# Kernel tuning notes

Hardware: AMD Instinct MI355X
Metric: run time of the kernel (lower is better)

## Reference

```python
import jax, jax.numpy as jnp
import numpy as np

N, B, T = 2048, 16, 256

def setup_inputs() -> dict:
    key = jax.random.key(0)
    k1, k2, k3, k4 = jax.random.split(key, 4)
    x = jax.random.normal(k1, (B, T, N), dtype=jnp.float32)
    weight = jax.random.normal(k2, (T, T), dtype=jnp.float32) * (1.0 / np.sqrt(T))
    bias = jax.random.normal(k3, (T,), dtype=jnp.float32) * 0.01
    # Gumbel(0,1) noise, matching torch.nn.functional.gumbel_softmax internals
    u = jax.random.uniform(k4, (N * N, 2), dtype=jnp.float32, minval=1e-6, maxval=1.0 - 1e-6)
    gumbel = -jnp.log(-jnp.log(u))
    return {"x": x, "weight": weight, "bias": bias, "gumbel": gumbel}

def reference(x, weight, bias, gumbel):
    # x: [B, T, N] -> node-major [N, B, T]
    xp = jnp.transpose(x, (2, 0, 1))
    n = xp.shape[0]
    # --- similarity-based logits (torch writes via .data -> no grad path) ---
    xs = jax.lax.stop_gradient(xp)
    x_avg = xs.mean(axis=1)                                          # [N, T]
    x_norm = x_avg / jnp.maximum(jnp.linalg.norm(x_avg, axis=-1, keepdims=True), 1e-12)
    sim = (x_norm @ x_norm.T + 1.0) * 0.5                            # [N, N] in [0,1]
    sim_flat = sim.reshape(-1)
    # gumbel_softmax(hard=True) forward: adjacency = argmax over (logits + g)
    score0 = sim_flat + gumbel[:, 0]
    score1 = (1.0 - sim_flat) + gumbel[:, 1]
    adj = (score0 > score1).astype(xp.dtype).reshape(n, n)           # directed adjacency
    # --- structural coefficient (dense, faithful to compute_structural_coeff) ---
    adj_sym = jnp.clip(adj + adj.T, 0.0, 1.0)
    nmask = jnp.clip(adj_sym + jnp.eye(n, dtype=xp.dtype), 0.0, 1.0)
    common = nmask @ nmask.T                                         # common-neighbor counts
    max_common = common.max()                                        # >= 1 (diagonal)
    valid = (adj_sym * (common > 1.0).astype(xp.dtype)) > 0
    struct = jnp.where(valid, (common / max_common) * common, 0.0)   # lambda_val = 1.0
    # edge weights only at directed-edge positions
    W = adj * struct                                                 # [src, dst]
    # --- gcn_norm (no self loops, improved=False): deg over dst, D^-1/2 W D^-1/2 ---
    deg = W.sum(axis=0)
    dinv = jnp.where(deg > 0, deg ** -0.5, 0.0)
    Wn = dinv[:, None] * W * dinv[None, :]
    # --- linear + gather-multiply-scatter aggregation (out[d] = sum_s Wn[s,d] x[s]) ---
    xw = jnp.einsum('nbt,to->nbo', xp, weight)                       # [N, B, T]
    out = jnp.einsum('sd,sbt->dbt', Wn, xw) + bias                   # [N, B, T]
    return jnp.transpose(out, (1, 2, 0))                             # [B, T, N]
```

## Files before the change

### kernel.cpp

```cpp
#include <hip/hip_runtime.h>

#define NN 2048
#define BB 16
#define TT 256

typedef unsigned short ushort_t;
typedef short bf16x8 __attribute__((ext_vector_type(8)));
typedef float f32x4 __attribute__((ext_vector_type(4)));

__device__ __forceinline__ ushort_t f2bf(float f) {
    unsigned u = __float_as_uint(f);
    return (ushort_t)((u + 0x7FFFu + ((u >> 16) & 1u)) >> 16);
}

__device__ __forceinline__ void gload16(const void* g, void* l) {
    __builtin_amdgcn_global_load_lds((const __attribute__((address_space(1))) unsigned int*)g,
                                     (__attribute__((address_space(3))) unsigned int*)l,
                                     16, 0, 0);
}

__global__ __launch_bounds__(256) void k_colsum(const float* __restrict__ x,
                                                float* __restrict__ xsumT,
                                                float* __restrict__ ssq) {
    const int n = blockIdx.x * 256 + threadIdx.x;
    const int t = blockIdx.y;
    float s = 0.f;
#pragma unroll
    for (int b = 0; b < BB; b++) s += x[(size_t)(b * TT + t) * NN + n];
    xsumT[(size_t)t * NN + n] = s;
    atomicAdd(&ssq[n], s * s);
}

__global__ __launch_bounds__(256) void k_adj(const float* __restrict__ A,
                                             const float* __restrict__ ssq,
                                             const float* __restrict__ gumbel,
                                             ushort_t* __restrict__ adjb) {
    __shared__ __align__(16) float As[8][128];
    __shared__ __align__(16) float Bs[8][128];
    const int m0 = blockIdx.y * 128, n0 = blockIdx.x * 128;
    const int tid = threadIdx.x;
    const int tx = tid & 15, ty = tid >> 4;
    const int lr = tid >> 5, lc = (tid & 31) * 4;
    float acc[8][8];
#pragma unroll
    for (int i = 0; i < 8; i++)
#pragma unroll
        for (int j = 0; j < 8; j++) acc[i][j] = 0.f;
    for (int k0 = 0; k0 < TT; k0 += 8) {
        __syncthreads();
        gload16(&A[(size_t)(k0 + lr) * NN + m0 + lc], &As[lr][lc]);
        gload16(&A[(size_t)(k0 + lr) * NN + n0 + lc], &Bs[lr][lc]);
        __syncthreads();
#pragma unroll
        for (int kk = 0; kk < 8; kk++) {
            float a[8], b[8];
            *(float4*)&a[0] = *(const float4*)&As[kk][ty * 8];
            *(float4*)&a[4] = *(const float4*)&As[kk][ty * 8 + 4];
            *(float4*)&b[0] = *(const float4*)&Bs[kk][tx * 8];
            *(float4*)&b[4] = *(const float4*)&Bs[kk][tx * 8 + 4];
#pragma unroll
            for (int i = 0; i < 8; i++)
#pragma unroll
                for (int j = 0; j < 8; j++) acc[i][j] = fmaf(a[i], b[j], acc[i][j]);
        }
    }
#pragma unroll
    for (int i = 0; i < 8; i++) {
        const int gi = m0 + ty * 8 + i;
        const float si = ssq[gi];
        const float invi = (si > 0.f) ? rsqrtf(si) : 0.f;
#pragma unroll
        for (int j = 0; j < 8; j++) {
            const int gj = n0 + tx * 8 + j;
            const float sj = ssq[gj];
            const float invj = (sj > 0.f) ? rsqrtf(sj) : 0.f;
            const float dot = acc[i][j] * invi * invj;
            const size_t fl = (size_t)gi * NN + gj;
            const float2 g = *(const float2*)&gumbel[2 * fl];
            adjb[fl] = (dot > g.y - g.x) ? (ushort_t)0x3F80 : (ushort_t)0;
        }
    }
}

__global__ __launch_bounds__(256) void k_nmask(const ushort_t* __restrict__ adjb,
                                               ushort_t* __restrict__ nm) {
    __shared__ ushort_t tt[32][33];
    const int J = blockIdx.x * 32, I = blockIdx.y * 32;
    const int c = threadIdx.x & 31, r0 = threadIdx.x >> 5;
#pragma unroll
    for (int r = r0; r < 32; r += 8) tt[r][c] = adjb[(size_t)(J + r) * NN + I + c];
    __syncthreads();
#pragma unroll
    for (int r = r0; r < 32; r += 8) {
        const int gi = I + r, gj = J + c;
        const bool on = (gi == gj) || adjb[(size_t)gi * NN + gj] || tt[c][r];
        nm[(size_t)gi * NN + gj] = on ? (ushort_t)0x3F80 : (ushort_t)0;
    }
}

__global__ __launch_bounds__(256) void k_commonW(const ushort_t* __restrict__ nm,
                                                 const ushort_t* __restrict__ adjb,
                                                 float* __restrict__ W,
                                                 float* __restrict__ deg) {
    __shared__ __align__(16) ushort_t As[128][32];
    __shared__ __align__(16) ushort_t Bs[128][32];
    const int m0 = blockIdx.y * 128, n0 = blockIdx.x * 128;
    const int tid = threadIdx.x;
    const int lane = tid & 63, wave = tid >> 6;
    const int wr = wave >> 1, wc = wave & 1;
    f32x4 acc[4][4];
#pragma unroll
    for (int i = 0; i < 4; i++)
#pragma unroll
        for (int j = 0; j < 4; j++) acc[i][j] = (f32x4){0.f, 0.f, 0.f, 0.f};
    const int r0 = tid >> 2, kc = (tid & 3) * 8;
    for (int k0 = 0; k0 < NN; k0 += 32) {
        __syncthreads();
        gload16(&nm[(size_t)(m0 + r0) * NN + k0 + kc], &As[r0][kc]);
        gload16(&nm[(size_t)(n0 + r0) * NN + k0 + kc], &Bs[r0][kc]);
        gload16(&nm[(size_t)(m0 + r0 + 64) * NN + k0 + kc], &As[r0 + 64][kc]);
        gload16(&nm[(size_t)(n0 + r0 + 64) * NN + k0 + kc], &Bs[r0 + 64][kc]);
        __syncthreads();
        const int lr = lane & 15, kg = (lane >> 4) * 8;
        bf16x8 af[4], bff[4];
#pragma unroll
        for (int f = 0; f < 4; f++) {
            af[f]  = *(const bf16x8*)&As[wr * 64 + f * 16 + lr][kg];
            bff[f] = *(const bf16x8*)&Bs[wc * 64 + f * 16 + lr][kg];
        }
#pragma unroll
        for (int i = 0; i < 4; i++)
#pragma unroll
            for (int j = 0; j < 4; j++)
                acc[i][j] = __builtin_amdgcn_mfma_f32_16x16x32_bf16(af[i], bff[j], acc[i][j], 0, 0, 0);
    }
    const int lr = lane & 15, rg = (lane >> 4) * 4;
#pragma unroll
    for (int j = 0; j < 4; j++) {
        const int gj = n0 + wc * 64 + j * 16 + lr;
        float psum = 0.f;
#pragma unroll
        for (int i = 0; i < 4; i++)
#pragma unroll
            for (int r = 0; r < 4; r++) {
                const int gi = m0 + wr * 64 + i * 16 + rg + r;
                const float cv = acc[i][j][r];
                const size_t fl = (size_t)gi * NN + gj;
                const float wv = (cv > 1.0f && adjb[fl]) ? cv * cv : 0.f;
                W[fl] = wv;
                psum += wv;
            }
        atomicAdd(&deg[gj], psum);
    }
}

__global__ __launch_bounds__(256) void k_wtn(const float* __restrict__ W,
                                             const float* __restrict__ deg,
                                             ushort_t* __restrict__ Wtn) {
    __shared__ float tt[64][65];
    const int S0 = blockIdx.x * 64, D0 = blockIdx.y * 64;
    const int c = threadIdx.x & 63, r0 = threadIdx.x >> 6;
#pragma unroll
    for (int r = r0; r < 64; r += 4) tt[r][c] = W[(size_t)(S0 + r) * NN + D0 + c];
    __syncthreads();
    const float dgs = deg[S0 + c];
    const float ds = (dgs > 0.f) ? rsqrtf(dgs) : 0.f;
#pragma unroll
    for (int r = r0; r < 64; r += 4) {
        const int d = D0 + r;
        const float dgd = deg[d];
        const float dd = (dgd > 0.f) ? rsqrtf(dgd) : 0.f;
        Wtn[(size_t)d * NN + S0 + c] = f2bf(tt[c][r] * ds * dd);
    }
}

__global__ __launch_bounds__(256) void k_xt(const float* __restrict__ x,
                                            ushort_t* __restrict__ xT) {
    __shared__ float tile[64][65];
    const int b = blockIdx.z, t0 = blockIdx.y * 64, n0 = blockIdx.x * 64;
    const int c = threadIdx.x & 63, r0 = threadIdx.x >> 6;
#pragma unroll
    for (int r = r0; r < 64; r += 4)
        tile[r][c] = x[(size_t)(b * TT + t0 + r) * NN + n0 + c];
    __syncthreads();
#pragma unroll
    for (int r = r0; r < 64; r += 4)
        xT[(size_t)(b * NN + n0 + r) * TT + t0 + c] = f2bf(tile[c][r]);
}

__global__ __launch_bounds__(256) void k_wt(const float* __restrict__ w,
                                            ushort_t* __restrict__ wT) {
    __shared__ float tile[64][65];
    const int t0 = blockIdx.y * 64, o0 = blockIdx.x * 64;
    const int c = threadIdx.x & 63, r0 = threadIdx.x >> 6;
#pragma unroll
    for (int r = r0; r < 64; r += 4)
        tile[r][c] = w[(size_t)(t0 + r) * TT + o0 + c];
    __syncthreads();
#pragma unroll
    for (int r = r0; r < 64; r += 4)
        wT[(size_t)(o0 + r) * TT + t0 + c] = f2bf(tile[c][r]);
}

__global__ __launch_bounds__(256) void k_xw(const ushort_t* __restrict__ wT,
                                            const ushort_t* __restrict__ xT,
                                            ushort_t* __restrict__ xwT) {
    __shared__ __align__(16) ushort_t As[128][32];
    __shared__ __align__(16) ushort_t Bs[128][32];
    const int b = blockIdx.z;
    const ushort_t* __restrict__ Bg = xT + (size_t)b * NN * TT;
    const int m0 = blockIdx.y * 128, n0 = blockIdx.x * 128;
    const int tid = threadIdx.x;
    const int lane = tid & 63, wave = tid >> 6;
    const int wr = wave >> 1, wc = wave & 1;
    f32x4 acc[4][4];
#pragma unroll
    for (int i = 0; i < 4; i++)
#pragma unroll
        for (int j = 0; j < 4; j++) acc[i][j] = (f32x4){0.f, 0.f, 0.f, 0.f};
    const int r0 = tid >> 2, kc = (tid & 3) * 8;
    for (int k0 = 0; k0 < TT; k0 += 32) {
        __syncthreads();
        gload16(&wT[(size_t)(m0 + r0) * TT + k0 + kc], &As[r0][kc]);
        gload16(&Bg[(size_t)(n0 + r0) * TT + k0 + kc], &Bs[r0][kc]);
        gload16(&wT[(size_t)(m0 + r0 + 64) * TT + k0 + kc], &As[r0 + 64][kc]);
        gload16(&Bg[(size_t)(n0 + r0 + 64) * TT + k0 + kc], &Bs[r0 + 64][kc]);
        __syncthreads();
        const int lr = lane & 15, kg = (lane >> 4) * 8;
        bf16x8 af[4], bff[4];
#pragma unroll
        for (int f = 0; f < 4; f++) {
            af[f]  = *(const bf16x8*)&As[wr * 64 + f * 16 + lr][kg];
            bff[f] = *(const bf16x8*)&Bs[wc * 64 + f * 16 + lr][kg];
        }
#pragma unroll
        for (int i = 0; i < 4; i++)
#pragma unroll
            for (int j = 0; j < 4; j++)
                acc[i][j] = __builtin_amdgcn_mfma_f32_16x16x32_bf16(af[i], bff[j], acc[i][j], 0, 0, 0);
    }
    const int lr = lane & 15, rg = (lane >> 4) * 4;
#pragma unroll
    for (int i = 0; i < 4; i++)
#pragma unroll
        for (int j = 0; j < 4; j++)
#pragma unroll
            for (int r = 0; r < 4; r++) {
                const int o = m0 + wr * 64 + i * 16 + rg + r;
                const int n = n0 + wc * 64 + j * 16 + lr;
                xwT[((size_t)b * TT + o) * NN + n] = f2bf(acc[i][j][r]);
            }
}

__global__ __launch_bounds__(256) void k_out(const ushort_t* __restrict__ xwT,
                                             const ushort_t* __restrict__ Wtn,
                                             const float* __restrict__ bias,
                                             float* __restrict__ out) {
    __shared__ __align__(16) ushort_t As[128][32];
    __shared__ __align__(16) ushort_t Bs[128][32];
    const int m0 = blockIdx.y * 128, n0 = blockIdx.x * 128;
    const int tid = threadIdx.x;
    const int lane = tid & 63, wave = tid >> 6;
    const int wr = wave >> 1, wc = wave & 1;
    f32x4 acc[4][4];
#pragma unroll
    for (int i = 0; i < 4; i++)
#pragma unroll
        for (int j = 0; j < 4; j++) acc[i][j] = (f32x4){0.f, 0.f, 0.f, 0.f};
    const int r0 = tid >> 2, kc = (tid & 3) * 8;
    for (int k0 = 0; k0 < NN; k0 += 32) {
        __syncthreads();
        gload16(&xwT[(size_t)(m0 + r0) * NN + k0 + kc], &As[r0][kc]);
        gload16(&Wtn[(size_t)(n0 + r0) * NN + k0 + kc], &Bs[r0][kc]);
        gload16(&xwT[(size_t)(m0 + r0 + 64) * NN + k0 + kc], &As[r0 + 64][kc]);
        gload16(&Wtn[(size_t)(n0 + r0 + 64) * NN + k0 + kc], &Bs[r0 + 64][kc]);
        __syncthreads();
        const int lr = lane & 15, kg = (lane >> 4) * 8;
        bf16x8 af[4], bff[4];
#pragma unroll
        for (int f = 0; f < 4; f++) {
            af[f]  = *(const bf16x8*)&As[wr * 64 + f * 16 + lr][kg];
            bff[f] = *(const bf16x8*)&Bs[wc * 64 + f * 16 + lr][kg];
        }
#pragma unroll
        for (int i = 0; i < 4; i++)
#pragma unroll
            for (int j = 0; j < 4; j++)
                acc[i][j] = __builtin_amdgcn_mfma_f32_16x16x32_bf16(af[i], bff[j], acc[i][j], 0, 0, 0);
    }
    const int lr = lane & 15, rg = (lane >> 4) * 4;
#pragma unroll
    for (int i = 0; i < 4; i++)
#pragma unroll
        for (int j = 0; j < 4; j++)
#pragma unroll
            for (int r = 0; r < 4; r++) {
                const int gm = m0 + wr * 64 + i * 16 + rg + r;
                const int gd = n0 + wc * 64 + j * 16 + lr;
                out[(size_t)gm * NN + gd] = acc[i][j][r] + bias[gm & (TT - 1)];
            }
}

extern "C" void kernel_launch(void* const* d_in, const int* in_sizes, int n_in,
                              void* d_out, int out_size, void* d_ws, size_t ws_size,
                              hipStream_t stream) {
    const float* x      = (const float*)d_in[0];
    const float* w      = (const float*)d_in[1];
    const float* bias   = (const float*)d_in[2];
    const float* gumbel = (const float*)d_in[3];
    float* out = (float*)d_out;

    char* ws = (char*)d_ws;
    float*    xsumT = (float*)(ws + 0);
    float*    ssq   = (float*)(ws + 2097152);
    float*    deg   = (float*)(ws + 2105344);
    ushort_t* adjb  = (ushort_t*)(ws + 2113536);
    ushort_t* nm    = (ushort_t*)(ws + 10502144);
    ushort_t* xT    = (ushort_t*)(ws + 2113536);
    float*    W     = (float*)(ws + 18890752);
    ushort_t* xwT   = (ushort_t*)(ws + 18890752);
    ushort_t* Wtn   = (ushort_t*)(ws + 35667968);
    ushort_t* wT    = (ushort_t*)(ws + 44056576);

    hipMemsetAsync(ws + 2097152, 0, 16384, stream);

    k_colsum <<<dim3(NN / 256, TT), 256, 0, stream>>>(x, xsumT, ssq);
    k_adj    <<<dim3(16, 16),       256, 0, stream>>>(xsumT, ssq, gumbel, adjb);
    k_nmask  <<<dim3(64, 64),       256, 0, stream>>>(adjb, nm);
    k_commonW<<<dim3(16, 16),       256, 0, stream>>>(nm, adjb, W, deg);
    k_wtn    <<<dim3(32, 32),       256, 0, stream>>>(W, deg, Wtn);
    k_xt     <<<dim3(32, 4, BB),    256, 0, stream>>>(x, xT);
    k_wt     <<<dim3(4, 4),         256, 0, stream>>>(w, wT);
    k_xw     <<<dim3(16, 2, BB),    256, 0, stream>>>(wT, xT, xwT);
    k_out    <<<dim3(16, 32),       256, 0, stream>>>(xwT, Wtn, bias, out);
}
```

Before: 308.2 us.

## Double-buffer LDS tiles in GEMM kernels and retile adjacency kernel to 64x64

```diff
diff --git a/kernel.cpp b/kernel.cpp
--- a/kernel.cpp
+++ b/kernel.cpp
@@ -17,6 +17,47 @@
     __builtin_amdgcn_global_load_lds((const __attribute__((address_space(1))) unsigned int*)g,
                                      (__attribute__((address_space(3))) unsigned int*)l,
                                      16, 0, 0);
+}
+
+__device__ __forceinline__ void mfma_loop128(
+    const ushort_t* __restrict__ Ag, size_t lda,
+    const ushort_t* __restrict__ Bg, size_t ldb,
+    int m0, int n0, int nkt,
+    ushort_t (*As)[128][32], ushort_t (*Bs)[128][32],
+    f32x4 (&acc)[4][4], int tid)
+{
+    const int lane = tid & 63, wave = tid >> 6;
+    const int wr = wave >> 1, wc = wave & 1;
+    const int r0 = tid >> 2, kc = (tid & 3) * 8;
+    const int lr = lane & 15, kg = (lane >> 4) * 8;
+    gload16(&Ag[(size_t)(m0 + r0) * lda + kc], &As[0][r0][kc]);
+    gload16(&Bg[(size_t)(n0 + r0) * ldb + kc], &Bs[0][r0][kc]);
+    gload16(&Ag[(size_t)(m0 + r0 + 64) * lda + kc], &As[0][r0 + 64][kc]);
+    gload16(&Bg[(size_t)(n0 + r0 + 64) * ldb + kc], &Bs[0][r0 + 64][kc]);
+    __syncthreads();
+    int cur = 0;
+    for (int kt = 0; kt < nkt; kt++) {
+        if (kt + 1 < nkt) {
+            const int k0 = (kt + 1) * 32;
+            gload16(&Ag[(size_t)(m0 + r0) * lda + k0 + kc], &As[cur ^ 1][r0][kc]);
+            gload16(&Bg[(size_t)(n0 + r0) * ldb + k0 + kc], &Bs[cur ^ 1][r0][kc]);
+            gload16(&Ag[(size_t)(m0 + r0 + 64) * lda + k0 + kc], &As[cur ^ 1][r0 + 64][kc]);
+            gload16(&Bg[(size_t)(n0 + r0 + 64) * ldb + k0 + kc], &Bs[cur ^ 1][r0 + 64][kc]);
+        }
+        bf16x8 af[4], bf[4];
+#pragma unroll
+        for (int f = 0; f < 4; f++) {
+            af[f] = *(const bf16x8*)&As[cur][wr * 64 + f * 16 + lr][kg];
+            bf[f] = *(const bf16x8*)&Bs[cur][wc * 64 + f * 16 + lr][kg];
+        }
+#pragma unroll
+        for (int i = 0; i < 4; i++)
+#pragma unroll
+            for (int j = 0; j < 4; j++)
+                acc[i][j] = __builtin_amdgcn_mfma_f32_16x16x32_bf16(af[i], bf[j], acc[i][j], 0, 0, 0);
+        __syncthreads();
+        cur ^= 1;
+    }
 }
 
 __global__ __launch_bounds__(256) void k_colsum(const float* __restrict__ x,
@@ -35,49 +76,62 @@
                                              const float* __restrict__ ssq,
                                              const float* __restrict__ gumbel,
                                              ushort_t* __restrict__ adjb) {
-    __shared__ __align__(16) float As[8][128];
-    __shared__ __align__(16) float Bs[8][128];
-    const int m0 = blockIdx.y * 128, n0 = blockIdx.x * 128;
+    __shared__ __align__(16) float As[2][32][64];
+    __shared__ __align__(16) float Bs[2][32][64];
+    const int m0 = blockIdx.y * 64, n0 = blockIdx.x * 64;
     const int tid = threadIdx.x;
     const int tx = tid & 15, ty = tid >> 4;
-    const int lr = tid >> 5, lc = (tid & 31) * 4;
-    float acc[8][8];
-#pragma unroll
-    for (int i = 0; i < 8; i++)
-#pragma unroll
-        for (int j = 0; j < 8; j++) acc[i][j] = 0.f;
-    for (int k0 = 0; k0 < TT; k0 += 8) {
+    const int sr = tid >> 4, sc = (tid & 15) * 4;
+    float acc[4][4];
+#pragma unroll
+    for (int i = 0; i < 4; i++)
+#pragma unroll
+        for (int j = 0; j < 4; j++) acc[i][j] = 0.f;
+    gload16(&A[(size_t)sr * NN + m0 + sc], &As[0][sr][sc]);
+    gload16(&A[(size_t)sr * NN + n0 + sc], &Bs[0][sr][sc]);
+    gload16(&A[(size_t)(sr + 16) * NN + m0 + sc], &As[0][sr + 16][sc]);
+    gload16(&A[(size_t)(sr + 16) * NN + n0 + sc], &Bs[0][sr + 16][sc]);
+    __syncthreads();
+    int cur = 0;
+    for (int kt = 0; kt < 8; kt++) {
+        if (kt + 1 < 8) {
+            const int k0 = (kt + 1) * 32;
+            gload16(&A[(size_t)(k0 + sr) * NN + m0 + sc], &As[cur ^ 1][sr][sc]);
+            gload16(&A[(size_t)(k0 + sr) * NN + n0 + sc], &Bs[cur ^ 1][sr][sc]);
+            gload16(&A[(size_t)(k0 + sr + 16) * NN + m0 + sc], &As[cur ^ 1][sr + 16][sc]);
+            gload16(&A[(size_t)(k0 + sr + 16) * NN + n0 + sc], &Bs[cur ^ 1][sr + 16][sc]);
+        }
+#pragma unroll 16
+        for (int kk = 0; kk < 32; kk++) {
+            float4 a = *(const float4*)&As[cur][kk][ty * 4];
+            float4 b = *(const float4*)&Bs[cur][kk][tx * 4];
+            const float av[4] = {a.x, a.y, a.z, a.w};
+            const float bv[4] = {b.x, b.y, b.z, b.w};
+#pragma unroll
+            for (int i = 0; i < 4; i++)
+#pragma unroll
+                for (int j = 0; j < 4; j++) acc[i][j] = fmaf(av[i], bv[j], acc[i][j]);
+        }
         __syncthreads();
-        gload16(&A[(size_t)(k0 + lr) * NN + m0 + lc], &As[lr][lc]);
-        gload16(&A[(size_t)(k0 + lr) * NN + n0 + lc], &Bs[lr][lc]);
-        __syncthreads();
-#pragma unroll
-        for (int kk = 0; kk < 8; kk++) {
-            float a[8], b[8];
-            *(float4*)&a[0] = *(const float4*)&As[kk][ty * 8];
-            *(float4*)&a[4] = *(const float4*)&As[kk][ty * 8 + 4];
-            *(float4*)&b[0] = *(const float4*)&Bs[kk][tx * 8];
-            *(float4*)&b[4] = *(const float4*)&Bs[kk][tx * 8 + 4];
-#pragma unroll
-            for (int i = 0; i < 8; i++)
-#pragma unroll
-                for (int j = 0; j < 8; j++) acc[i][j] = fmaf(a[i], b[j], acc[i][j]);
-        }
-    }
-#pragma unroll
-    for (int i = 0; i < 8; i++) {
-        const int gi = m0 + ty * 8 + i;
-        const float si = ssq[gi];
-        const float invi = (si > 0.f) ? rsqrtf(si) : 0.f;
-#pragma unroll
-        for (int j = 0; j < 8; j++) {
-            const int gj = n0 + tx * 8 + j;
-            const float sj = ssq[gj];
-            const float invj = (sj > 0.f) ? rsqrtf(sj) : 0.f;
-            const float dot = acc[i][j] * invi * invj;
-            const size_t fl = (size_t)gi * NN + gj;
-            const float2 g = *(const float2*)&gumbel[2 * fl];
-            adjb[fl] = (dot > g.y - g.x) ? (ushort_t)0x3F80 : (ushort_t)0;
+        cur ^= 1;
+    }
+    float invi[4], invj[4];
+#pragma unroll
+    for (int i = 0; i < 4; i++) {
+        const float si = ssq[m0 + ty * 4 + i];
+        invi[i] = (si > 0.f) ? rsqrtf(si) : 0.f;
+        const float sj = ssq[n0 + tx * 4 + i];
+        invj[i] = (sj > 0.f) ? rsqrtf(sj) : 0.f;
+    }
+#pragma unroll
+    for (int i = 0; i < 4; i++) {
+        const int gi = m0 + ty * 4 + i;
+        const size_t rowb = (size_t)gi * NN + n0 + tx * 4;
+#pragma unroll
+        for (int j = 0; j < 4; j++) {
+            const float dot = acc[i][j] * invi[i] * invj[j];
+            const float2 g = *(const float2*)&gumbel[2 * (rowb + j)];
+            adjb[rowb + j] = (dot > g.y - g.x) ? (ushort_t)0x3F80 : (ushort_t)0;
         }
     }
 }
@@ -102,8 +156,8 @@
                                                  const ushort_t* __restrict__ adjb,
                                                  float* __restrict__ W,
                                                  float* __restrict__ deg) {
-    __shared__ __align__(16) ushort_t As[128][32];
-    __shared__ __align__(16) ushort_t Bs[128][32];
+    __shared__ __align__(16) ushort_t As[2][128][32];
+    __shared__ __align__(16) ushort_t Bs[2][128][32];
     const int m0 = blockIdx.y * 128, n0 = blockIdx.x * 128;
     const int tid = threadIdx.x;
     const int lane = tid & 63, wave = tid >> 6;
@@ -113,27 +167,7 @@
     for (int i = 0; i < 4; i++)
 #pragma unroll
         for (int j = 0; j < 4; j++) acc[i][j] = (f32x4){0.f, 0.f, 0.f, 0.f};
-    const int r0 = tid >> 2, kc = (tid & 3) * 8;
-    for (int k0 = 0; k0 < NN; k0 += 32) {
-        __syncthreads();
-        gload16(&nm[(size_t)(m0 + r0) * NN + k0 + kc], &As[r0][kc]);
-        gload16(&nm[(size_t)(n0 + r0) * NN + k0 + kc], &Bs[r0][kc]);
-        gload16(&nm[(size_t)(m0 + r0 + 64) * NN + k0 + kc], &As[r0 + 64][kc]);
-        gload16(&nm[(size_t)(n0 + r0 + 64) * NN + k0 + kc], &Bs[r0 + 64][kc]);
-        __syncthreads();
-        const int lr = lane & 15, kg = (lane >> 4) * 8;
-        bf16x8 af[4], bff[4];
-#pragma unroll
-        for (int f = 0; f < 4; f++) {
-            af[f]  = *(const bf16x8*)&As[wr * 64 + f * 16 + lr][kg];
-            bff[f] = *(const bf16x8*)&Bs[wc * 64 + f * 16 + lr][kg];
-        }
-#pragma unroll
-        for (int i = 0; i < 4; i++)
-#pragma unroll
-            for (int j = 0; j < 4; j++)
-                acc[i][j] = __builtin_amdgcn_mfma_f32_16x16x32_bf16(af[i], bff[j], acc[i][j], 0, 0, 0);
-    }
+    mfma_loop128(nm, NN, nm, NN, m0, n0, NN / 32, As, Bs, acc, tid);
     const int lr = lane & 15, rg = (lane >> 4) * 4;
 #pragma unroll
     for (int j = 0; j < 4; j++) {
@@ -205,8 +239,8 @@
 __global__ __launch_bounds__(256) void k_xw(const ushort_t* __restrict__ wT,
                                             const ushort_t* __restrict__ xT,
                                             ushort_t* __restrict__ xwT) {
-    __shared__ __align__(16) ushort_t As[128][32];
-    __shared__ __align__(16) ushort_t Bs[128][32];
+    __shared__ __align__(16) ushort_t As[2][128][32];
+    __shared__ __align__(16) ushort_t Bs[2][128][32];
     const int b = blockIdx.z;
     const ushort_t* __restrict__ Bg = xT + (size_t)b * NN * TT;
     const int m0 = blockIdx.y * 128, n0 = blockIdx.x * 128;
@@ -218,27 +252,7 @@
     for (int i = 0; i < 4; i++)
 #pragma unroll
         for (int j = 0; j < 4; j++) acc[i][j] = (f32x4){0.f, 0.f, 0.f, 0.f};
-    const int r0 = tid >> 2, kc = (tid & 3) * 8;
-    for (int k0 = 0; k0 < TT; k0 += 32) {
-        __syncthreads();
-        gload16(&wT[(size_t)(m0 + r0) * TT + k0 + kc], &As[r0][kc]);
-        gload16(&Bg[(size_t)(n0 + r0) * TT + k0 + kc], &Bs[r0][kc]);
-        gload16(&wT[(size_t)(m0 + r0 + 64) * TT + k0 + kc], &As[r0 + 64][kc]);
-        gload16(&Bg[(size_t)(n0 + r0 + 64) * TT + k0 + kc], &Bs[r0 + 64][kc]);
-        __syncthreads();
-        const int lr = lane & 15, kg = (lane >> 4) * 8;
-        bf16x8 af[4], bff[4];
-#pragma unroll
-        for (int f = 0; f < 4; f++) {
-            af[f]  = *(const bf16x8*)&As[wr * 64 + f * 16 + lr][kg];
-            bff[f] = *(const bf16x8*)&Bs[wc * 64 + f * 16 + lr][kg];
-        }
-#pragma unroll
-        for (int i = 0; i < 4; i++)
-#pragma unroll
-            for (int j = 0; j < 4; j++)
-                acc[i][j] = __builtin_amdgcn_mfma_f32_16x16x32_bf16(af[i], bff[j], acc[i][j], 0, 0, 0);
-    }
+    mfma_loop128(wT, TT, Bg, TT, m0, n0, TT / 32, As, Bs, acc, tid);
     const int lr = lane & 15, rg = (lane >> 4) * 4;
 #pragma unroll
     for (int i = 0; i < 4; i++)
@@ -256,8 +270,8 @@
                                              const ushort_t* __restrict__ Wtn,
                                              const float* __restrict__ bias,
                                              float* __restrict__ out) {
-    __shared__ __align__(16) ushort_t As[128][32];
-    __shared__ __align__(16) ushort_t Bs[128][32];
+    __shared__ __align__(16) ushort_t As[2][128][32];
+    __shared__ __align__(16) ushort_t Bs[2][128][32];
     const int m0 = blockIdx.y * 128, n0 = blockIdx.x * 128;
     const int tid = threadIdx.x;
     const int lane = tid & 63, wave = tid >> 6;
@@ -267,27 +281,7 @@
     for (int i = 0; i < 4; i++)
 #pragma unroll
         for (int j = 0; j < 4; j++) acc[i][j] = (f32x4){0.f, 0.f, 0.f, 0.f};
-    const int r0 = tid >> 2, kc = (tid & 3) * 8;
-    for (int k0 = 0; k0 < NN; k0 += 32) {
-        __syncthreads();
-        gload16(&xwT[(size_t)(m0 + r0) * NN + k0 + kc], &As[r0][kc]);
-        gload16(&Wtn[(size_t)(n0 + r0) * NN + k0 + kc], &Bs[r0][kc]);
-        gload16(&xwT[(size_t)(m0 + r0 + 64) * NN + k0 + kc], &As[r0 + 64][kc]);
-        gload16(&Wtn[(size_t)(n0 + r0 + 64) * NN + k0 + kc], &Bs[r0 + 64][kc]);
-        __syncthreads();
-        const int lr = lane & 15, kg = (lane >> 4) * 8;
-        bf16x8 af[4], bff[4];
-#pragma unroll
-        for (int f = 0; f < 4; f++) {
-            af[f]  = *(const bf16x8*)&As[wr * 64 + f * 16 + lr][kg];
-            bff[f] = *(const bf16x8*)&Bs[wc * 64 + f * 16 + lr][kg];
-        }
-#pragma unroll
-        for (int i = 0; i < 4; i++)
-#pragma unroll
-            for (int j = 0; j < 4; j++)
-                acc[i][j] = __builtin_amdgcn_mfma_f32_16x16x32_bf16(af[i], bff[j], acc[i][j], 0, 0, 0);
-    }
+    mfma_loop128(xwT, NN, Wtn, NN, m0, n0, NN / 32, As, Bs, acc, tid);
     const int lr = lane & 15, rg = (lane >> 4) * 4;
 #pragma unroll
     for (int i = 0; i < 4; i++)
@@ -325,7 +319,7 @@
     hipMemsetAsync(ws + 2097152, 0, 16384, stream);
 
     k_colsum <<<dim3(NN / 256, TT), 256, 0, stream>>>(x, xsumT, ssq);
-    k_adj    <<<dim3(16, 16),       256, 0, stream>>>(xsumT, ssq, gumbel, adjb);
+    k_adj    <<<dim3(32, 32),       256, 0, stream>>>(xsumT, ssq, gumbel, adjb);
     k_nmask  <<<dim3(64, 64),       256, 0, stream>>>(adjb, nm);
     k_commonW<<<dim3(16, 16),       256, 0, stream>>>(nm, adjb, W, deg);
     k_wtn    <<<dim3(32, 32),       256, 0, stream>>>(W, deg, Wtn);
```

Result: no change. 310.9 us (+0.9%).
